# Optimization experiments

Measured on AMD Instinct MI355X. Metric: run time of the kernel, lower is better.

The kernel has to match this reference:

```python
import jax, jax.numpy as jnp
import numpy as np

NUM_HEADS = 16
LN_EPS = 1e-5


def _transpose_qkv(X, num_heads):
    # Faithful to the repo's (buggy) transpose_qkv:
    # (B,S,D) -> (B,S,H,D/H) -> permute (B,H,S,D/H) -> reshape (B,S,D)
    B, S, D = X.shape
    X = X.reshape(B, S, num_heads, D // num_heads)
    X = jnp.transpose(X, (0, 2, 1, 3))
    return X.reshape(B, S, D)


def _layer_norm(x, w, b):
    mu = jnp.mean(x, axis=-1, keepdims=True)
    var = jnp.var(x, axis=-1, keepdims=True)
    return (x - mu) * jax.lax.rsqrt(var + LN_EPS) * w + b


def setup_inputs() -> dict:
    key = jax.random.key(0)
    ks = jax.random.split(key, 4)
    B, S, D = 4, 2048, 1024
    scale = 1.0 / np.sqrt(D)
    return {
        "src": jax.random.normal(ks[0], (B, S, D), dtype=jnp.float32),
        "W_q": jax.random.normal(ks[1], (D, D), dtype=jnp.float32) * scale,
        "W_k": jax.random.normal(ks[2], (D, D), dtype=jnp.float32) * scale,
        "W_v": jax.random.normal(ks[3], (D, D), dtype=jnp.float32) * scale,
        "ln1_w": jnp.ones((D,), dtype=jnp.float32),
        "ln1_b": jnp.zeros((D,), dtype=jnp.float32),
        "ln2_w": jnp.ones((D,), dtype=jnp.float32),
        "ln2_b": jnp.zeros((D,), dtype=jnp.float32),
    }


def reference(src, W_q, W_k, W_v, ln1_w, ln1_b, ln2_w, ln2_b):
    # W_* stored as (in, out): y = x @ W  (equivalent to torch Linear, bias=False)
    q = _transpose_qkv(src @ W_q, NUM_HEADS)  # (B,S,D)
    k = _transpose_qkv(src @ W_k, NUM_HEADS)
    v = _transpose_qkv(src @ W_v, NUM_HEADS)
    d = q.shape[-1]  # note: full hidden dim, per the buggy transpose_qkv
    scores = jnp.einsum("bqd,bkd->bqk", q, k) / jnp.sqrt(jnp.float32(d))
    a = jax.nn.softmax(scores, axis=-1)          # (B,S,S) attention weights
    att = jnp.einsum("bqk,bkd->bqd", a, v)       # (B,S,D)
    src2 = _layer_norm(att, ln1_w, ln1_b)        # norm1
    X = _layer_norm(src + src2, ln2_w, ln2_b)    # AddNorm (dropout=0 in eval)
    return (X, a)
```

## Files before the change

### kernel.cpp

```cpp
#include <hip/hip_runtime.h>

typedef _Float16 f16;
typedef __attribute__((ext_vector_type(2))) _Float16 f16x2;
typedef __attribute__((ext_vector_type(4))) _Float16 f16x4;
typedef __attribute__((ext_vector_type(8))) _Float16 f16x8;
typedef __attribute__((ext_vector_type(4))) float f32x4;

#define D_MODEL 1024
#define SEQ 2048
#define NBATCH 4
#define NROWS (NBATCH * SEQ)

__device__ __forceinline__ void gload16(const void* g, void* l) {
  __builtin_amdgcn_global_load_lds(
      (__attribute__((address_space(1))) void*)(void*)g,
      (__attribute__((address_space(3))) void*)l, 16, 0, 0);
}

#define BAR __builtin_amdgcn_s_barrier()
#define LGK0                                              \
  asm volatile("s_waitcnt lgkmcnt(0)" ::: "memory");      \
  __builtin_amdgcn_sched_barrier(0)
#define PRIO1 __builtin_amdgcn_s_setprio(1)
#define PRIO0 __builtin_amdgcn_s_setprio(0)

template <int BN>
__device__ __forceinline__ void gemm8_core(
    const f16* aP0, const f16* aP1, const f16* aP2, const f16* aP3,
    const f16* bP0, const f16* bP1, const f16* bP2, const f16* bP3,
    int stepA, int stepB, int NT, f16* lds, f32x4* acc)
{
  constexpr int NJ = BN / 128;
  constexpr int NACC = 2 * NJ;
  constexpr int SLOT = 16384 + BN * 64;
  const int t = threadIdx.x, l = t & 63;
  const int w = t >> 6, wm = w >> 2, wn = w & 3;
  const int fr = l & 15, g0 = l >> 4;

  int aof[2][4][2], bof[2][NJ][2];
#pragma unroll
  for (int mh = 0; mh < 2; ++mh)
#pragma unroll
    for (int mi = 0; mi < 4; ++mi)
#pragma unroll
      for (int kh = 0; kh < 2; ++kh) {
        const int ra = wm * 128 + mh * 64 + mi * 16 + fr;
        aof[mh][mi][kh] = ra * 64 + (((g0 + kh * 4) ^ (ra & 7)) << 3);
      }
#pragma unroll
  for (int nh = 0; nh < 2; ++nh)
#pragma unroll
    for (int j = 0; j < NJ; ++j)
#pragma unroll
      for (int kh = 0; kh < 2; ++kh) {
        const int rb = (BN == 256) ? (wn * 64 + fr * 4 + nh * 2 + j)
                                   : (wn * 32 + fr * 2 + nh);
        bof[nh][j][kh] = rb * 64 + (((g0 + kh * 4) ^ ((rb >> 2) & 7)) << 3);
      }
#pragma unroll
  for (int i = 0; i < 8 * NACC; ++i) acc[i] = f32x4{0.f, 0.f, 0.f, 0.f};

  f16x8 fa[4][2];
  f16x8 fb[2][NJ][2];

#define STAGE_A(SL)                                  \
  {                                                  \
    f16* d = lds + (SL) * SLOT + t * 8;              \
    gload16(aP0, d);                                 \
    gload16(aP1, d + 4096);                          \
    gload16(aP2, d + 8192);                          \
    gload16(aP3, d + 12288);                         \
  }
#define STAGE_B(SL)                                  \
  {                                                  \
    f16* d = lds + (SL) * SLOT + 16384 + t * 8;      \
    gload16(bP0, d);                                 \
    gload16(bP1, d + 4096);                          \
    if constexpr (BN == 256) {                       \
      gload16(bP2, d + 8192);                        \
      gload16(bP3, d + 12288);                       \
    }                                                \
  }
#define ADV                                          \
  aP0 += stepA; aP1 += stepA; aP2 += stepA; aP3 += stepA; \
  bP0 += stepB; bP1 += stepB;                        \
  if constexpr (BN == 256) { bP2 += stepB; bP3 += stepB; }
#define VMC                                                        \
  if constexpr (BN == 256) {                                       \
    asm volatile("s_waitcnt vmcnt(8)" ::: "memory");               \
  } else {                                                         \
    asm volatile("s_waitcnt vmcnt(6)" ::: "memory");               \
  }
#define LOAD_A(MH)                                   \
  _Pragma("unroll") for (int mi = 0; mi < 4; ++mi)   \
  _Pragma("unroll") for (int kh = 0; kh < 2; ++kh)   \
      fa[mi][kh] = *(const f16x8*)(LA + aof[MH][mi][kh]);
#define LOAD_B(NH)                                   \
  _Pragma("unroll") for (int j = 0; j < NJ; ++j)     \
  _Pragma("unroll") for (int kh = 0; kh < 2; ++kh)   \
      fb[NH][j][kh] = *(const f16x8*)(LB + bof[NH][j][kh]);
#define MFMA_BLK(MH, NH)                                                    \
  _Pragma("unroll") for (int mi = 0; mi < 4; ++mi)                          \
  _Pragma("unroll") for (int j = 0; j < NJ; ++j)                            \
  _Pragma("unroll") for (int kh = 0; kh < 2; ++kh)                          \
      acc[((MH)*4 + mi) * NACC + (NH)*NJ + j] =                             \
          __builtin_amdgcn_mfma_f32_16x16x32_f16(                           \
              fa[mi][kh], fb[NH][j][kh],                                    \
              acc[((MH)*4 + mi) * NACC + (NH)*NJ + j], 0, 0, 0);

  (void)bP2; (void)bP3;
  STAGE_A(0); STAGE_B(0); ADV;
  STAGE_A(1); STAGE_B(1); ADV;
  VMC;
  BAR;

  for (int kt = 0; kt < NT; ++kt) {
    const int sl = kt & 1;
    const f16* LA = lds + sl * SLOT;
    const f16* LB = LA + 16384;
    LOAD_A(0); LOAD_B(0);
    BAR; LGK0;
    PRIO1; MFMA_BLK(0, 0); PRIO0; BAR;
    LOAD_B(1);
    BAR; LGK0;
    PRIO1; MFMA_BLK(0, 1); PRIO0; BAR;
    LOAD_A(1);
    STAGE_B(sl);
    BAR; LGK0;
    PRIO1; MFMA_BLK(1, 0); PRIO0; BAR;
    STAGE_A(sl);
    if (kt + 3 < NT) { ADV; }
    VMC;
    BAR;
    PRIO1; MFMA_BLK(1, 1); PRIO0; BAR;
  }
#undef STAGE_A
#undef STAGE_B
#undef ADV
#undef VMC
#undef LOAD_A
#undef LOAD_B
#undef MFMA_BLK
}

__global__ __launch_bounds__(512, 2) void k_qkv3(
    const f16* __restrict__ srch, const f16* __restrict__ wt,
    f16* __restrict__ qp, f16* __restrict__ kp, f16* __restrict__ vp)
{
  __shared__ f16 lds[2 * (16384 + 256 * 64)];
  const int t = threadIdx.x, l = t & 63;
  const int w = t >> 6, wm = w >> 2, wn = w & 3;
  const int fr = l & 15, g0 = l >> 4, c = t & 7;
  const f16 *aP[4], *bP[4];
#pragma unroll
  for (int i = 0; i < 4; ++i) {
    const int rl = i * 64 + (t >> 3);
    aP[i] = srch + (size_t)(blockIdx.x * 256 + rl) * 1024 + ((c ^ (rl & 7)) << 3);
    bP[i] = wt + (size_t)(blockIdx.y * 256 + rl) * 1024 + ((c ^ ((rl >> 2) & 7)) << 3);
  }
  f32x4 acc[32];
  gemm8_core<256>(aP[0], aP[1], aP[2], aP[3], bP[0], bP[1], bP[2], bP[3],
                  64, 64, 16, lds, acc);
  const int z = blockIdx.y >> 2;
  f16* dst = (z == 0) ? qp : (z == 1 ? kp : vp);
  const int col = (blockIdx.y & 3) * 256 + wn * 64 + fr * 4;
#pragma unroll
  for (int mi = 0; mi < 8; ++mi)
#pragma unroll
    for (int q = 0; q < 4; ++q) {
      const int row = blockIdx.x * 256 + wm * 128 + mi * 16 + g0 * 4 + q;
      f16x4 o = {(f16)acc[mi * 4 + 0][q], (f16)acc[mi * 4 + 1][q],
                 (f16)acc[mi * 4 + 2][q], (f16)acc[mi * 4 + 3][q]};
      *(f16x4*)(dst + (size_t)row * 1024 + col) = o;
    }
}

__global__ __launch_bounds__(512, 2) void k_scores(
    const f16* __restrict__ qp, const f16* __restrict__ kp,
    f16* __restrict__ abf)
{
  __shared__ f16 lds[2 * (16384 + 256 * 64)];
  const int t = threadIdx.x, l = t & 63;
  const int w = t >> 6, wm = w >> 2, wn = w & 3;
  const int fr = l & 15, g0 = l >> 4, c = t & 7;
  const int b = blockIdx.z;
  const f16* qb = qp + ((size_t)b << 21);
  const f16* kb = kp + ((size_t)b << 21);
  const f16 *aP[4], *bP[4];
#pragma unroll
  for (int i = 0; i < 4; ++i) {
    const int rl = i * 64 + (t >> 3);
    const int spA = blockIdx.x * 256 + rl;
    aP[i] = qb + (size_t)((spA & 127) << 4) * 1024 + ((spA >> 7) << 6) +
            ((c ^ (rl & 7)) << 3);
    const int spB = blockIdx.y * 256 + rl;
    bP[i] = kb + (size_t)((spB & 127) << 4) * 1024 + ((spB >> 7) << 6) +
            ((c ^ ((rl >> 2) & 7)) << 3);
  }
  f32x4 acc[32];
  gemm8_core<256>(aP[0], aP[1], aP[2], aP[3], bP[0], bP[1], bP[2], bP[3],
                  1024, 1024, 16, lds, acc);
  f16* Cb = abf + ((size_t)b << 22);
  const int col = blockIdx.y * 256 + wn * 64 + fr * 4;
#pragma unroll
  for (int mi = 0; mi < 8; ++mi)
#pragma unroll
    for (int q = 0; q < 4; ++q) {
      const int row = blockIdx.x * 256 + wm * 128 + mi * 16 + g0 * 4 + q;
      f16x4 o = {(f16)(acc[mi * 4 + 0][q] * 0.03125f),
                 (f16)(acc[mi * 4 + 1][q] * 0.03125f),
                 (f16)(acc[mi * 4 + 2][q] * 0.03125f),
                 (f16)(acc[mi * 4 + 3][q] * 0.03125f)};
      *(f16x4*)(Cb + (size_t)row * 2048 + col) = o;
    }
}

__global__ __launch_bounds__(512, 2) void k_att(
    const f16* __restrict__ abf, const f16* __restrict__ vtT,
    f16* __restrict__ attb)
{
  __shared__ f16 lds[2 * (16384 + 128 * 64)];
  const int t = threadIdx.x, l = t & 63;
  const int w = t >> 6, wm = w >> 2, wn = w & 3;
  const int fr = l & 15, g0 = l >> 4, c = t & 7;
  const int b = blockIdx.z;
  const f16* ab = abf + ((size_t)b << 22);
  const f16* vb = vtT + ((size_t)b << 21);
  const f16 *aP[4], *bP[2];
#pragma unroll
  for (int i = 0; i < 4; ++i) {
    const int rl = i * 64 + (t >> 3);
    aP[i] = ab + (size_t)(blockIdx.x * 256 + rl) * 2048 + ((c ^ (rl & 7)) << 3);
  }
#pragma unroll
  for (int i = 0; i < 2; ++i) {
    const int rl = i * 64 + (t >> 3);
    bP[i] = vb + (size_t)(blockIdx.y * 128 + rl) * 2048 +
            ((c ^ ((rl >> 2) & 7)) << 3);
  }
  f32x4 acc[16];
  gemm8_core<128>(aP[0], aP[1], aP[2], aP[3], bP[0], bP[1], bP[0], bP[0],
                  64, 64, 32, lds, acc);
  f16* Cb = attb + ((size_t)b << 21);
  const int col = blockIdx.y * 128 + wn * 32 + fr * 2;
#pragma unroll
  for (int mi = 0; mi < 8; ++mi)
#pragma unroll
    for (int q = 0; q < 4; ++q) {
      const int row = blockIdx.x * 256 + wm * 128 + mi * 16 + g0 * 4 + q;
      f16x2 o = {(f16)acc[mi * 2 + 0][q], (f16)acc[mi * 2 + 1][q]};
      *(f16x2*)(Cb + (size_t)row * 1024 + col) = o;
    }
}

__global__ __launch_bounds__(256) void k_scrT(const f16* __restrict__ vp,
                                              f16* __restrict__ vtT)
{
  __shared__ f16 tile[64][68];
  const int t = threadIdx.x;
  const int sp0 = blockIdx.x * 64, dp0 = blockIdx.y * 64;
  const int d6 = dp0 >> 6;
  const int jb = (sp0 >> 7) << 6;
  const int sbase = sp0 & 127;
  const f16* src = vp + ((size_t)blockIdx.z << 21);
  f16* dst = vtT + ((size_t)blockIdx.z << 21);
#pragma unroll
  for (int p = 0; p < 2; ++p) {
    const int u = p * 32 + (t >> 3);
    const int s = ((sbase + u) << 4) | d6;
    const int c = (t & 7) << 3;
    f16x8 v = *(const f16x8*)(src + (size_t)s * 1024 + jb + c);
    *(f16x4*)&tile[u][c]     = f16x4{v[0], v[1], v[2], v[3]};
    *(f16x4*)&tile[u][c + 4] = f16x4{v[4], v[5], v[6], v[7]};
  }
  __syncthreads();
#pragma unroll
  for (int p = 0; p < 2; ++p) {
    const int cc = p * 32 + (t >> 3);
    const int v0 = (t & 7) << 3;
    f16x8 o;
#pragma unroll
    for (int j = 0; j < 8; ++j) o[j] = tile[v0 + j][cc];
    *(f16x8*)(dst + (size_t)(dp0 + cc) * 2048 + sp0 + v0) = o;
  }
}

__global__ __launch_bounds__(256) void k_cast_f16(const float* __restrict__ in,
                                                  f16* __restrict__ out)
{
  const size_t i = (size_t)blockIdx.x * 256 + threadIdx.x;
  const float4* p = (const float4*)in;
  float4 v0 = p[2 * i], v1 = p[2 * i + 1];
  f16x8 o;
  o[0] = (f16)v0.x; o[1] = (f16)v0.y; o[2] = (f16)v0.z; o[3] = (f16)v0.w;
  o[4] = (f16)v1.x; o[5] = (f16)v1.y; o[6] = (f16)v1.z; o[7] = (f16)v1.w;
  *(f16x8*)(out + 8 * i) = o;
}

__global__ __launch_bounds__(256) void k_castT(
    const float* __restrict__ w0, const float* __restrict__ w1,
    const float* __restrict__ w2, f16* __restrict__ out)
{
  const float* in = (blockIdx.z == 0) ? w0 : (blockIdx.z == 1 ? w1 : w2);
  f16* o = out + ((size_t)blockIdx.z << 20);
  __shared__ f16 tile[64][65];
  const int t = threadIdx.x;
  const int rr = t >> 4, c4 = (t & 15) * 4;
  const int r0 = blockIdx.x * 64, c0 = blockIdx.y * 64;
#pragma unroll
  for (int i = 0; i < 4; ++i) {
    float4 f = *(const float4*)(in + (size_t)(r0 + rr + 16 * i) * 1024 + c0 + c4);
    tile[rr + 16 * i][c4 + 0] = (f16)f.x;
    tile[rr + 16 * i][c4 + 1] = (f16)f.y;
    tile[rr + 16 * i][c4 + 2] = (f16)f.z;
    tile[rr + 16 * i][c4 + 3] = (f16)f.w;
  }
  __syncthreads();
#pragma unroll
  for (int i = 0; i < 4; ++i) {
    const int n = c0 + rr + 16 * i;
    f16* dst = o + (size_t)n * 1024 + r0 + c4;
    dst[0] = tile[c4 + 0][rr + 16 * i];
    dst[1] = tile[c4 + 1][rr + 16 * i];
    dst[2] = tile[c4 + 2][rr + 16 * i];
    dst[3] = tile[c4 + 3][rr + 16 * i];
  }
}

__global__ __launch_bounds__(256) void k_softmax(float* __restrict__ out,
                                                 f16* __restrict__ abf)
{
  const size_t base = (size_t)blockIdx.x * 2048;
  const int t = threadIdx.x, lane = t & 63, w = t >> 6;
  f16x8 v = *(const f16x8*)(abf + base + (size_t)t * 8);
  float x[8];
#pragma unroll
  for (int j = 0; j < 8; ++j) x[j] = (float)v[j];
  float m = fmaxf(fmaxf(fmaxf(x[0], x[1]), fmaxf(x[2], x[3])),
                  fmaxf(fmaxf(x[4], x[5]), fmaxf(x[6], x[7])));
#pragma unroll
  for (int off = 1; off < 64; off <<= 1) m = fmaxf(m, __shfl_xor(m, off));
  __shared__ float red[8];
  if (lane == 0) red[w] = m;
  __syncthreads();
  m = fmaxf(fmaxf(red[0], red[1]), fmaxf(red[2], red[3]));
  float s = 0.f;
#pragma unroll
  for (int j = 0; j < 8; ++j) { x[j] = __expf(x[j] - m); s += x[j]; }
#pragma unroll
  for (int off = 1; off < 64; off <<= 1) s += __shfl_xor(s, off);
  if (lane == 0) red[4 + w] = s;
  __syncthreads();
  s = red[4] + red[5] + red[6] + red[7];
  const float inv = 1.0f / s;
#pragma unroll
  for (int j = 0; j < 8; ++j) x[j] *= inv;
  float4 o0 = {x[0], x[1], x[2], x[3]}, o1 = {x[4], x[5], x[6], x[7]};
  ((float4*)(out + base))[2 * t] = o0;
  ((float4*)(out + base))[2 * t + 1] = o1;
  f16x8 ov;
#pragma unroll
  for (int j = 0; j < 8; ++j) ov[j] = (f16)x[j];
  *(f16x8*)(abf + base + (size_t)t * 8) = ov;
}

__global__ __launch_bounds__(256) void k_ln(
    const f16* __restrict__ attb, const float* __restrict__ src,
    const float* __restrict__ w1, const float* __restrict__ b1,
    const float* __restrict__ w2, const float* __restrict__ b2,
    float* __restrict__ out)
{
  const size_t base = (size_t)blockIdx.x * 1024;
  const int t = threadIdx.x, lane = t & 63, w = t >> 6;
  f16x4 a4 = ((const f16x4*)(attb + base))[t];
  float ax = (float)a4[0], ay = (float)a4[1], az = (float)a4[2], aw = (float)a4[3];
  float s = ax + ay + az + aw;
  float s2 = ax * ax + ay * ay + az * az + aw * aw;
#pragma unroll
  for (int off = 1; off < 64; off <<= 1) {
    s += __shfl_xor(s, off);
    s2 += __shfl_xor(s2, off);
  }
  __shared__ float red[16];
  if (lane == 0) { red[w] = s; red[4 + w] = s2; }
  __syncthreads();
  s = red[0] + red[1] + red[2] + red[3];
  s2 = red[4] + red[5] + red[6] + red[7];
  float mu = s * (1.0f / 1024.0f);
  float var = s2 * (1.0f / 1024.0f) - mu * mu;
  float rs = rsqrtf(var + 1e-5f);
  float4 W1 = ((const float4*)w1)[t], B1 = ((const float4*)b1)[t];
  float4 sv = ((const float4*)(src + base))[t];
  float y0 = sv.x + (ax - mu) * rs * W1.x + B1.x;
  float y1 = sv.y + (ay - mu) * rs * W1.y + B1.y;
  float y2 = sv.z + (az - mu) * rs * W1.z + B1.z;
  float y3 = sv.w + (aw - mu) * rs * W1.w + B1.w;
  s = y0 + y1 + y2 + y3;
  s2 = y0 * y0 + y1 * y1 + y2 * y2 + y3 * y3;
#pragma unroll
  for (int off = 1; off < 64; off <<= 1) {
    s += __shfl_xor(s, off);
    s2 += __shfl_xor(s2, off);
  }
  if (lane == 0) { red[8 + w] = s; red[12 + w] = s2; }
  __syncthreads();
  s = red[8] + red[9] + red[10] + red[11];
  s2 = red[12] + red[13] + red[14] + red[15];
  mu = s * (1.0f / 1024.0f);
  var = s2 * (1.0f / 1024.0f) - mu * mu;
  rs = rsqrtf(var + 1e-5f);
  float4 W2 = ((const float4*)w2)[t], B2 = ((const float4*)b2)[t];
  float4 o;
  o.x = (y0 - mu) * rs * W2.x + B2.x;
  o.y = (y1 - mu) * rs * W2.y + B2.y;
  o.z = (y2 - mu) * rs * W2.z + B2.z;
  o.w = (y3 - mu) * rs * W2.w + B2.w;
  ((float4*)(out + base))[t] = o;
}

extern "C" void kernel_launch(void* const* d_in, const int* in_sizes, int n_in,
                              void* d_out, int out_size, void* d_ws, size_t ws_size,
                              hipStream_t stream) {
  const float* src = (const float*)d_in[0];
  const float* Wq  = (const float*)d_in[1];
  const float* Wk  = (const float*)d_in[2];
  const float* Wv  = (const float*)d_in[3];
  const float* l1w = (const float*)d_in[4];
  const float* l1b = (const float*)d_in[5];
  const float* l2w = (const float*)d_in[6];
  const float* l2b = (const float*)d_in[7];
  float* Xout = (float*)d_out;
  float* Aout = Xout + (size_t)NROWS * D_MODEL;

  char* ws = (char*)d_ws;
  f16* srch = (f16*)ws;
  f16* wt   = (f16*)(ws + (16u << 20));
  f16* qp   = (f16*)(ws + (22u << 20));
  f16* kp   = (f16*)(ws + (38u << 20));
  f16* vp   = (f16*)(ws + (54u << 20));
  f16* vtT  = (f16*)(ws + (70u << 20));
  f16* abf  = (f16*)(ws + (86u << 20));
  f16* attb = (f16*)(ws + (118u << 20));

  k_cast_f16<<<4096, 256, 0, stream>>>(src, srch);
  k_castT<<<dim3(16, 16, 3), 256, 0, stream>>>(Wq, Wk, Wv, wt);
  k_qkv3<<<dim3(32, 12), 512, 0, stream>>>(srch, wt, qp, kp, vp);
  k_scrT<<<dim3(32, 16, 4), 256, 0, stream>>>(vp, vtT);
  k_scores<<<dim3(8, 8, 4), 512, 0, stream>>>(qp, kp, abf);
  k_softmax<<<NROWS, 256, 0, stream>>>(Aout, abf);
  k_att<<<dim3(8, 8, 4), 512, 0, stream>>>(abf, vtT, attb);
  k_ln<<<NROWS, 256, 0, stream>>>(attb, src, l1w, l1b, l2w, l2b, Xout);
}
```

Measured before the change: 209.1 us.

## Restructure GEMM core pipeline and shrink QKV projection tile to 256x128

Rewrites the shared GEMM main loop: the A tile for the next slot is staged at the start of each iteration, both N-halves of MFMAs are fused into one block with a single barrier per half, and the explicit lgkmcnt waits are removed. The vmcnt thresholds change to match the new load ordering. The QKV projection kernel moves from 256x256 tiles to 256x128 tiles, doubling its grid so more blocks can fill the CUs. The trade-off is fewer barriers and more load/compute overlap against less B reuse per block, plus narrower f16x2 output stores. Dropping the lgkmcnt waits leaves LDS read ordering to the compiler, which is a correctness risk.

```diff
diff --git a/kernel.cpp b/kernel.cpp
--- a/kernel.cpp
+++ b/kernel.cpp
@@ -17,10 +17,12 @@
       (__attribute__((address_space(3))) void*)l, 16, 0, 0);
 }
 
-#define BAR __builtin_amdgcn_s_barrier()
-#define LGK0                                              \
-  asm volatile("s_waitcnt lgkmcnt(0)" ::: "memory");      \
-  __builtin_amdgcn_sched_barrier(0)
+#define BARF                                   \
+  do {                                         \
+    asm volatile("" ::: "memory");             \
+    __builtin_amdgcn_s_barrier();              \
+    asm volatile("" ::: "memory");             \
+  } while (0)
 #define PRIO1 __builtin_amdgcn_s_setprio(1)
 #define PRIO0 __builtin_amdgcn_s_setprio(0)
 
@@ -81,15 +83,17 @@
       gload16(bP3, d + 12288);                       \
     }                                                \
   }
-#define ADV                                          \
-  aP0 += stepA; aP1 += stepA; aP2 += stepA; aP3 += stepA; \
-  bP0 += stepB; bP1 += stepB;                        \
-  if constexpr (BN == 256) { bP2 += stepB; bP3 += stepB; }
+#define ADVA { aP0 += stepA; aP1 += stepA; aP2 += stepA; aP3 += stepA; }
+#define ADVB                                         \
+  {                                                  \
+    bP0 += stepB; bP1 += stepB;                      \
+    if constexpr (BN == 256) { bP2 += stepB; bP3 += stepB; } \
+  }
 #define VMC                                                        \
   if constexpr (BN == 256) {                                       \
-    asm volatile("s_waitcnt vmcnt(8)" ::: "memory");               \
+    asm volatile("s_waitcnt vmcnt(4)" ::: "memory");               \
   } else {                                                         \
-    asm volatile("s_waitcnt vmcnt(6)" ::: "memory");               \
+    asm volatile("s_waitcnt vmcnt(2)" ::: "memory");               \
   }
 #define LOAD_A(MH)                                   \
   _Pragma("unroll") for (int mi = 0; mi < 4; ++mi)   \
@@ -98,7 +102,7 @@
 #define LOAD_B(NH)                                   \
   _Pragma("unroll") for (int j = 0; j < NJ; ++j)     \
   _Pragma("unroll") for (int kh = 0; kh < 2; ++kh)   \
-      fb[NH][j][kh] = *(const f16x8*)(LB + bof[NH][j][kh]);
+      fb[NH][j][kh] = *(const f16x8*)(LBp + bof[NH][j][kh]);
 #define MFMA_BLK(MH, NH)                                                    \
   _Pragma("unroll") for (int mi = 0; mi < 4; ++mi)                          \
   _Pragma("unroll") for (int j = 0; j < NJ; ++j)                            \
@@ -109,34 +113,32 @@
               acc[((MH)*4 + mi) * NACC + (NH)*NJ + j], 0, 0, 0);
 
   (void)bP2; (void)bP3;
-  STAGE_A(0); STAGE_B(0); ADV;
-  STAGE_A(1); STAGE_B(1); ADV;
+  STAGE_A(0); ADVA;
+  STAGE_B(0); ADVB;
+  STAGE_B(1); ADVB;
   VMC;
-  BAR;
+  BARF;
 
   for (int kt = 0; kt < NT; ++kt) {
     const int sl = kt & 1;
     const f16* LA = lds + sl * SLOT;
-    const f16* LB = LA + 16384;
-    LOAD_A(0); LOAD_B(0);
-    BAR; LGK0;
-    PRIO1; MFMA_BLK(0, 0); PRIO0; BAR;
-    LOAD_B(1);
-    BAR; LGK0;
-    PRIO1; MFMA_BLK(0, 1); PRIO0; BAR;
+    const f16* LBp = LA + 16384;
+    STAGE_A(sl ^ 1);
+    if (kt + 2 < NT) ADVA;
+    LOAD_A(0); LOAD_B(0); LOAD_B(1);
+    PRIO1; MFMA_BLK(0, 0); MFMA_BLK(0, 1); PRIO0;
+    BARF;
     LOAD_A(1);
     STAGE_B(sl);
-    BAR; LGK0;
-    PRIO1; MFMA_BLK(1, 0); PRIO0; BAR;
-    STAGE_A(sl);
-    if (kt + 3 < NT) { ADV; }
+    if (kt + 3 < NT) ADVB;
     VMC;
-    BAR;
-    PRIO1; MFMA_BLK(1, 1); PRIO0; BAR;
+    PRIO1; MFMA_BLK(1, 0); MFMA_BLK(1, 1); PRIO0;
+    BARF;
   }
 #undef STAGE_A
 #undef STAGE_B
-#undef ADV
+#undef ADVA
+#undef ADVB
 #undef VMC
 #undef LOAD_A
 #undef LOAD_B
@@ -147,31 +149,35 @@
     const f16* __restrict__ srch, const f16* __restrict__ wt,
     f16* __restrict__ qp, f16* __restrict__ kp, f16* __restrict__ vp)
 {
-  __shared__ f16 lds[2 * (16384 + 256 * 64)];
+  __shared__ f16 lds[2 * (16384 + 128 * 64)];
   const int t = threadIdx.x, l = t & 63;
   const int w = t >> 6, wm = w >> 2, wn = w & 3;
   const int fr = l & 15, g0 = l >> 4, c = t & 7;
-  const f16 *aP[4], *bP[4];
+  const int z = blockIdx.y >> 3, cb = blockIdx.y & 7;
+  const f16 *aP[4], *bP[2];
 #pragma unroll
   for (int i = 0; i < 4; ++i) {
     const int rl = i * 64 + (t >> 3);
     aP[i] = srch + (size_t)(blockIdx.x * 256 + rl) * 1024 + ((c ^ (rl & 7)) << 3);
-    bP[i] = wt + (size_t)(blockIdx.y * 256 + rl) * 1024 + ((c ^ ((rl >> 2) & 7)) << 3);
-  }
-  f32x4 acc[32];
-  gemm8_core<256>(aP[0], aP[1], aP[2], aP[3], bP[0], bP[1], bP[2], bP[3],
+  }
+#pragma unroll
+  for (int i = 0; i < 2; ++i) {
+    const int rl = i * 64 + (t >> 3);
+    bP[i] = wt + ((size_t)z << 20) + (size_t)(cb * 128 + rl) * 1024 +
+            ((c ^ ((rl >> 2) & 7)) << 3);
+  }
+  f32x4 acc[16];
+  gemm8_core<128>(aP[0], aP[1], aP[2], aP[3], bP[0], bP[1], bP[0], bP[0],
                   64, 64, 16, lds, acc);
-  const int z = blockIdx.y >> 2;
   f16* dst = (z == 0) ? qp : (z == 1 ? kp : vp);
-  const int col = (blockIdx.y & 3) * 256 + wn * 64 + fr * 4;
+  const int col = cb * 128 + wn * 32 + fr * 2;
 #pragma unroll
   for (int mi = 0; mi < 8; ++mi)
 #pragma unroll
     for (int q = 0; q < 4; ++q) {
       const int row = blockIdx.x * 256 + wm * 128 + mi * 16 + g0 * 4 + q;
-      f16x4 o = {(f16)acc[mi * 4 + 0][q], (f16)acc[mi * 4 + 1][q],
-                 (f16)acc[mi * 4 + 2][q], (f16)acc[mi * 4 + 3][q]};
-      *(f16x4*)(dst + (size_t)row * 1024 + col) = o;
+      f16x2 o = {(f16)acc[mi * 2 + 0][q], (f16)acc[mi * 2 + 1][q]};
+      *(f16x2*)(dst + (size_t)row * 1024 + col) = o;
     }
 }
 
@@ -444,7 +450,7 @@
 
   k_cast_f16<<<4096, 256, 0, stream>>>(src, srch);
   k_castT<<<dim3(16, 16, 3), 256, 0, stream>>>(Wq, Wk, Wv, wt);
-  k_qkv3<<<dim3(32, 12), 512, 0, stream>>>(srch, wt, qp, kp, vp);
+  k_qkv3<<<dim3(32, 24), 512, 0, stream>>>(srch, wt, qp, kp, vp);
   k_scrT<<<dim3(32, 16, 4), 256, 0, stream>>>(vp, vtT);
   k_scores<<<dim3(8, 8, 4), 512, 0, stream>>>(qp, kp, abf);
   k_softmax<<<NROWS, 256, 0, stream>>>(Aout, abf);
```

After: 201.4 us. -3.7%, faster.
